# Performance work log

Hardware: AMD Instinct MI355X
Metric: run time of the kernel (lower is better)

## Reference

```python
import jax, jax.numpy as jnp
import numpy as np

B, S, D, H, DI, L = 16, 80, 512, 64, 2048, 6  # batch, seq, d_model, d_lstm(=d_v), d_inner, n_layers
EPS = 1e-6


def _layer_norm(x, g, b):
    m = jnp.mean(x, axis=-1, keepdims=True)
    v = jnp.mean((x - m) ** 2, axis=-1, keepdims=True)
    return (x - m) * jax.lax.rsqrt(v + EPS) * g + b


def _lstm_last(gx, whh):
    # gx: [T, N, 4H] precomputed input-to-gate projections (bias=False LSTM)
    N = gx.shape[1]
    Hh = whh.shape[1]
    init = (jnp.zeros((N, Hh), gx.dtype), jnp.zeros((N, Hh), gx.dtype))

    def step(carry, g_in):
        h, c = carry
        gates = g_in + h @ whh.T  # [N, 4H], torch gate order i,f,g,o
        i, f, g, o = jnp.split(gates, 4, axis=-1)
        c = jax.nn.sigmoid(f) * c + jax.nn.sigmoid(i) * jnp.tanh(g)
        h = jax.nn.sigmoid(o) * jnp.tanh(c)
        return (h, c), None

    (h, _), _ = jax.lax.scan(step, init, gx)
    return h  # [N, H]


def _perm_indices():
    # deterministic janossy permutation: identity with position i swapped to last
    idx = np.arange(S)
    P = np.tile(idx, (S, 1))
    P[idx, idx] = S - 1
    P[idx, S - 1] = idx
    return jnp.asarray(P)  # [S, S]


def _janossy_layer(q, g, b, wih, whh, wfc, P):
    # q: [B, S, D]
    x = _layer_norm(q, g, b)
    # project inputs to gates once, then gather permutations of the projection
    xg = jnp.einsum('bsd,gd->sbg', x, wih)  # [S, B, 4H]
    pg = xg[P]  # [S_i, S_t, B, 4H]: for each output position i, the permuted sequence
    pg = pg.transpose(1, 0, 2, 3).reshape(S, S * B, 4 * H)  # time-major, fold i into batch
    h = _lstm_last(pg, whh)  # [S*B, H]
    h = h.reshape(S, B, H).transpose(1, 0, 2)  # [B, S, H]
    return h @ wfc.T + q  # fc (dropout=identity in eval) + residual


def _ffn(q, g, b, w1, b1, w2, b2):
    x = _layer_norm(q, g, b)
    return jax.nn.relu(x @ w1.T + b1) @ w2.T + b2 + q


def setup_inputs() -> dict:
    key = jax.random.key(0)
    ks = jax.random.split(key, 10)
    n = lambda k, s, sc: jax.random.normal(k, s, jnp.float32) * sc
    return {
        'src_seq': jax.random.normal(ks[0], (B, S, D), jnp.float32),
        'trg_seq': jax.random.normal(ks[1], (B, S, D), jnp.float32),
        'ln1_g': jnp.ones((L, D), jnp.float32),
        'ln1_b': jnp.zeros((L, D), jnp.float32),
        'wih': n(ks[2], (L, 4 * H, D), 0.04),
        'whh': n(ks[3], (L, 4 * H, H), 0.1),
        'wfc': n(ks[4], (L, D, H), 0.05),
        'ln2_g': jnp.ones((L, D), jnp.float32),
        'ln2_b': jnp.zeros((L, D), jnp.float32),
        'w1': n(ks[5], (L, DI, D), 0.03),
        'b1': jnp.zeros((L, DI), jnp.float32),
        'w2': n(ks[6], (L, D, DI), 0.02),
        'b2': jnp.zeros((L, D), jnp.float32),
        'lnf_g': jnp.ones((D,), jnp.float32),
        'lnf_b': jnp.zeros((D,), jnp.float32),
        'wprj': n(ks[7], (1, D), 0.05),
    }


def reference(src_seq, trg_seq, ln1_g, ln1_b, wih, whh, wfc, ln2_g, ln2_b,
              w1, b1, w2, b2, lnf_g, lnf_b, wprj):
    P = _perm_indices()
    x = src_seq
    for l in range(L):  # small fixed layer count
        x = _janossy_layer(x, ln1_g[l], ln1_b[l], wih[l], whh[l], wfc[l], P)
        x = _ffn(x, ln2_g[l], ln2_b[l], w1[l], b1[l], w2[l], b2[l])
    x = _layer_norm(x, lnf_g, lnf_b)
    seq_logit = x @ wprj.T  # [B, S, 1]
    return seq_logit
```

## Files before the change

kernel.cpp:

```cpp
#include <hip/hip_runtime.h>
#include <hip/hip_bf16.h>

#define B_ 16
#define S_ 80
#define D_ 512
#define H_ 64
#define DI_ 2048
#define L_ 6
#define G4H 256
#define NROW (B_ * S_)
#define EPS_ 1e-6f

typedef __attribute__((ext_vector_type(8))) short short8;
typedef __attribute__((ext_vector_type(4))) float f32x4;

__device__ __forceinline__ float sigmoidf_(float x) {
    return __fdividef(1.0f, 1.0f + __expf(-x));
}
__device__ __forceinline__ float tanh_(float x) {
    return __fdividef(2.0f, 1.0f + __expf(-2.0f * x)) - 1.0f;
}
__device__ __forceinline__ short f2bf(float f) {
    __hip_bfloat16 h = __float2bfloat16(f);
    return *reinterpret_cast<short*>(&h);
}

__device__ __forceinline__ void lds_barrier() {
    __asm__ volatile("s_waitcnt lgkmcnt(0)\n\ts_barrier" ::: "memory");
}

__global__ __launch_bounds__(256)
void w2bf_kernel(const float* __restrict__ s, __hip_bfloat16* __restrict__ d, int n4) {
    int i = blockIdx.x * 256 + threadIdx.x;
    if (i < n4) {
        float4 v = reinterpret_cast<const float4*>(s)[i];
        short4 o;
        o.x = f2bf(v.x); o.y = f2bf(v.y); o.z = f2bf(v.z); o.w = f2bf(v.w);
        reinterpret_cast<short4*>(d)[i] = o;
    }
}

__global__ __launch_bounds__(256)
void ln_kernel(const float* __restrict__ x, const float* __restrict__ g,
               const float* __restrict__ b, __hip_bfloat16* __restrict__ out) {
    int row = blockIdx.x;
    int t = threadIdx.x;
    const float* xr = x + (size_t)row * D_;
    float v0 = xr[t], v1 = xr[t + 256];
    __shared__ float ws4[4], qs4[4];
    float s = v0 + v1;
    #pragma unroll
    for (int o = 32; o > 0; o >>= 1) s += __shfl_down(s, o);
    if ((t & 63) == 0) ws4[t >> 6] = s;
    __syncthreads();
    float m = (ws4[0] + ws4[1] + ws4[2] + ws4[3]) * (1.0f / (float)D_);
    float d0 = v0 - m, d1 = v1 - m;
    float q = d0 * d0 + d1 * d1;
    #pragma unroll
    for (int o = 32; o > 0; o >>= 1) q += __shfl_down(q, o);
    if ((t & 63) == 0) qs4[t >> 6] = q;
    __syncthreads();
    float rs = rsqrtf((qs4[0] + qs4[1] + qs4[2] + qs4[3]) * (1.0f / (float)D_) + EPS_);
    __hip_bfloat16* orow = out + (size_t)row * D_;
    orow[t]       = __float2bfloat16(d0 * rs * g[t]       + b[t]);
    orow[t + 256] = __float2bfloat16(d1 * rs * g[t + 256] + b[t + 256]);
}

template<int WITH_BIAS, int WITH_RELU, int WITH_RES, int OUT_MODE>
__global__ __launch_bounds__(256)
void mfma_gemm(const __hip_bfloat16* __restrict__ A, const __hip_bfloat16* __restrict__ W,
               const float* __restrict__ bias, const float* __restrict__ res,
               void* __restrict__ C, int M, int N, int K) {
    const int LDT = 72;
    __shared__ short As[64 * LDT];
    __shared__ short Ws[64 * LDT];

    int tid  = threadIdx.x;
    int wave = tid >> 6, lane = tid & 63;
    int quad = lane >> 4, l16 = lane & 15;
    int m_off = (wave >> 1) * 32, n_off = (wave & 1) * 32;
    int m0 = blockIdx.y * 64, n0 = blockIdx.x * 64;

    int r = tid >> 2, c = tid & 3;
    const short* Ag = reinterpret_cast<const short*>(A);
    const short* Wg = reinterpret_cast<const short*>(W);

    f32x4 acc00 = {0.f,0.f,0.f,0.f}, acc01 = acc00, acc10 = acc00, acc11 = acc00;

    short8 avA[2], avW[2];
    auto load_tile = [&](int k0) {
        const short* arow = &Ag[(size_t)(m0 + r) * K + k0 + c * 16];
        avA[0] = *reinterpret_cast<const short8*>(arow);
        avA[1] = *reinterpret_cast<const short8*>(arow + 8);
        const short* wrow = &Wg[(size_t)(n0 + r) * K + k0 + c * 16];
        avW[0] = *reinterpret_cast<const short8*>(wrow);
        avW[1] = *reinterpret_cast<const short8*>(wrow + 8);
    };

    load_tile(0);
    for (int k0 = 0; k0 < K; k0 += 64) {
        lds_barrier();
        *reinterpret_cast<short8*>(&As[r * LDT + c * 16])     = avA[0];
        *reinterpret_cast<short8*>(&As[r * LDT + c * 16 + 8]) = avA[1];
        *reinterpret_cast<short8*>(&Ws[r * LDT + c * 16])     = avW[0];
        *reinterpret_cast<short8*>(&Ws[r * LDT + c * 16 + 8]) = avW[1];
        lds_barrier();
        if (k0 + 64 < K) load_tile(k0 + 64);

        #pragma unroll
        for (int kc = 0; kc < 2; kc++) {
            short8 a0 = *reinterpret_cast<const short8*>(&As[(m_off + l16) * LDT + kc * 32 + quad * 8]);
            short8 a1 = *reinterpret_cast<const short8*>(&As[(m_off + 16 + l16) * LDT + kc * 32 + quad * 8]);
            short8 b0 = *reinterpret_cast<const short8*>(&Ws[(n_off + l16) * LDT + kc * 32 + quad * 8]);
            short8 b1 = *reinterpret_cast<const short8*>(&Ws[(n_off + 16 + l16) * LDT + kc * 32 + quad * 8]);
            acc00 = __builtin_amdgcn_mfma_f32_16x16x32_bf16(a0, b0, acc00, 0, 0, 0);
            acc01 = __builtin_amdgcn_mfma_f32_16x16x32_bf16(a0, b1, acc01, 0, 0, 0);
            acc10 = __builtin_amdgcn_mfma_f32_16x16x32_bf16(a1, b0, acc10, 0, 0, 0);
            acc11 = __builtin_amdgcn_mfma_f32_16x16x32_bf16(a1, b1, acc11, 0, 0, 0);
        }
    }

    f32x4 accs[2][2] = {{acc00, acc01}, {acc10, acc11}};
    #pragma unroll
    for (int fi = 0; fi < 2; fi++) {
        #pragma unroll
        for (int fj = 0; fj < 2; fj++) {
            int coln = n0 + n_off + fj * 16 + l16;
            float bv = WITH_BIAS ? bias[coln] : 0.0f;
            #pragma unroll
            for (int rr = 0; rr < 4; rr++) {
                int rowm = m0 + m_off + fi * 16 + quad * 4 + rr;
                float v = accs[fi][fj][rr];
                if (WITH_BIAS) v += bv;
                if (WITH_RELU) v = fmaxf(v, 0.0f);
                if (WITH_RES)  v += res[(size_t)rowm * N + coln];
                if (OUT_MODE == 0) {
                    reinterpret_cast<float*>(C)[(size_t)rowm * N + coln] = v;
                } else if (OUT_MODE == 1) {
                    reinterpret_cast<__hip_bfloat16*>(C)[(size_t)rowm * N + coln] = __float2bfloat16(v);
                } else {
                    int b_ = rowm / S_;
                    int s_ = rowm - b_ * S_;
                    int gate = coln >> 6, u = coln & 63;
                    int half = b_ >> 3, slot = b_ & 7;
                    reinterpret_cast<float*>(C)[
                        ((((size_t)(s_ * 2 + half) * 4 + gate) * 64 + u) << 3) + slot] = v;
                }
            }
        }
    }
}

__global__ __launch_bounds__(256)
void lstm_v10_kernel(const float* __restrict__ xg5,
                     const float* __restrict__ whh,
                     __hip_bfloat16* __restrict__ hlast) {
    const int i    = blockIdx.x;
    const int bh   = blockIdx.y;
    const int tid  = threadIdx.x;
    const int wave = tid >> 6, lane = tid & 63;
    const int quad = lane >> 4, l16 = lane & 15;
    const int unit = wave * 16 + l16;

    short8 bfrag[4][2];
    #pragma unroll
    for (int g = 0; g < 4; g++) {
        const float* wr = &whh[(size_t)(g * 64 + unit) * H_];
        #pragma unroll
        for (int kc = 0; kc < 2; kc++) {
            float4 x0 = *(const float4*)(wr + kc * 32 + quad * 8);
            float4 x1 = *(const float4*)(wr + kc * 32 + quad * 8 + 4);
            short8 v;
            v[0] = f2bf(x0.x); v[1] = f2bf(x0.y); v[2] = f2bf(x0.z); v[3] = f2bf(x0.w);
            v[4] = f2bf(x1.x); v[5] = f2bf(x1.y); v[6] = f2bf(x1.z); v[7] = f2bf(x1.w);
            bfrag[g][kc] = v;
        }
    }

    __shared__ __attribute__((aligned(16))) short hsh[2][16][72];
    for (int idx = tid; idx < 2 * 16 * 72; idx += 256)
        reinterpret_cast<short*>(hsh)[idx] = 0;

    float cst[2] = {0.f, 0.f};
    float hvv[2] = {0.f, 0.f};

    size_t xoff[4];
    #pragma unroll
    for (int g = 0; g < 4; g++)
        xoff[g] = ((((size_t)bh * 4 + g) * 64 + unit) << 3) + quad * 2;

    auto xload = [&](float2 (&xv)[4], int t) {
        int s = (t == i) ? (S_ - 1) : ((t == S_ - 1) ? i : t);
        const float* base = xg5 + (size_t)s * 4096;
        #pragma unroll
        for (int g = 0; g < 4; g++)
            xv[g] = *reinterpret_cast<const float2*>(base + xoff[g]);
    };

    float2 xvA[4], xvB[4];
    xload(xvA, 0);
    xload(xvB, 1);

    lds_barrier();

    const f32x4 zacc = {0.f, 0.f, 0.f, 0.f};

    auto stepv = [&](int t, float2 (&xc)[4]) {
        const int pb = t & 1;
        short8 af0 = *reinterpret_cast<const short8*>(&hsh[pb][l16][quad * 8]);
        short8 af1 = *reinterpret_cast<const short8*>(&hsh[pb][l16][32 + quad * 8]);

        f32x4 p0 = __builtin_amdgcn_mfma_f32_16x16x32_bf16(af0, bfrag[0][0], zacc, 0, 0, 0);
        f32x4 q0 = __builtin_amdgcn_mfma_f32_16x16x32_bf16(af1, bfrag[0][1], zacc, 0, 0, 0);
        f32x4 p1 = __builtin_amdgcn_mfma_f32_16x16x32_bf16(af0, bfrag[1][0], zacc, 0, 0, 0);
        f32x4 q1 = __builtin_amdgcn_mfma_f32_16x16x32_bf16(af1, bfrag[1][1], zacc, 0, 0, 0);
        f32x4 p2 = __builtin_amdgcn_mfma_f32_16x16x32_bf16(af0, bfrag[2][0], zacc, 0, 0, 0);
        f32x4 q2 = __builtin_amdgcn_mfma_f32_16x16x32_bf16(af1, bfrag[2][1], zacc, 0, 0, 0);
        f32x4 p3 = __builtin_amdgcn_mfma_f32_16x16x32_bf16(af0, bfrag[3][0], zacc, 0, 0, 0);
        f32x4 q3 = __builtin_amdgcn_mfma_f32_16x16x32_bf16(af1, bfrag[3][1], zacc, 0, 0, 0);

        float gi0 = p0[0] + q0[0] + xc[0].x, gi1 = p0[1] + q0[1] + xc[0].y;
        float gf0 = p1[0] + q1[0] + xc[1].x, gf1 = p1[1] + q1[1] + xc[1].y;
        float gg0 = p2[0] + q2[0] + xc[2].x, gg1 = p2[1] + q2[1] + xc[2].y;
        float go0 = p3[0] + q3[0] + xc[3].x, go1 = p3[1] + q3[1] + xc[3].y;

        if (t + 2 < S_) xload(xc, t + 2);

        {
            float ig = sigmoidf_(gi0);
            float fg = sigmoidf_(gf0);
            float gv = tanh_(gg0);
            float og = sigmoidf_(go0);
            float cc = fg * cst[0] + ig * gv;
            cst[0] = cc;
            float h = og * tanh_(cc);
            hvv[0] = h;
            hsh[pb ^ 1][quad * 4 + 0][unit] = f2bf(h);
        }
        {
            float ig = sigmoidf_(gi1);
            float fg = sigmoidf_(gf1);
            float gv = tanh_(gg1);
            float og = sigmoidf_(go1);
            float cc = fg * cst[1] + ig * gv;
            cst[1] = cc;
            float h = og * tanh_(cc);
            hvv[1] = h;
            hsh[pb ^ 1][quad * 4 + 1][unit] = f2bf(h);
        }
        lds_barrier();
    };

    for (int t = 0; t < S_; t += 2) { stepv(t, xvA); stepv(t + 1, xvB); }

    #pragma unroll
    for (int r = 0; r < 2; r++) {
        int b = bh * 8 + quad * 2 + r;
        hlast[((size_t)b * S_ + i) * H_ + unit] = __float2bfloat16(hvv[r]);
    }
}

__global__ __launch_bounds__(256)
void final_kernel(const float* __restrict__ x, const float* __restrict__ g,
                  const float* __restrict__ b, const float* __restrict__ wprj,
                  float* __restrict__ out) {
    int row = blockIdx.x;
    int t = threadIdx.x;
    const float* xr = x + (size_t)row * D_;
    float v0 = xr[t], v1 = xr[t + 256];
    __shared__ float red[256];
    red[t] = v0 + v1;
    __syncthreads();
    for (int o = 128; o > 0; o >>= 1) { if (t < o) red[t] += red[t + o]; __syncthreads(); }
    float m = red[0] * (1.0f / (float)D_);
    __syncthreads();
    float d0 = v0 - m, d1 = v1 - m;
    red[t] = d0 * d0 + d1 * d1;
    __syncthreads();
    for (int o = 128; o > 0; o >>= 1) { if (t < o) red[t] += red[t + o]; __syncthreads(); }
    float rs = rsqrtf(red[0] * (1.0f / (float)D_) + EPS_);
    __syncthreads();
    float y0 = (d0 * rs * g[t] + b[t]) * wprj[t];
    float y1 = (d1 * rs * g[t + 256] + b[t + 256]) * wprj[t + 256];
    red[t] = y0 + y1;
    __syncthreads();
    for (int o = 128; o > 0; o >>= 1) { if (t < o) red[t] += red[t + o]; __syncthreads(); }
    if (t == 0) out[row] = red[0];
}

extern "C" void kernel_launch(void* const* d_in, const int* in_sizes, int n_in,
                              void* d_out, int out_size, void* d_ws, size_t ws_size,
                              hipStream_t stream) {
    const float* src   = (const float*)d_in[0];
    const float* ln1_g = (const float*)d_in[2];
    const float* ln1_b = (const float*)d_in[3];
    const float* wih   = (const float*)d_in[4];
    const float* whh   = (const float*)d_in[5];
    const float* wfc   = (const float*)d_in[6];
    const float* ln2_g = (const float*)d_in[7];
    const float* ln2_b = (const float*)d_in[8];
    const float* w1    = (const float*)d_in[9];
    const float* b1    = (const float*)d_in[10];
    const float* w2    = (const float*)d_in[11];
    const float* b2    = (const float*)d_in[12];
    const float* lnf_g = (const float*)d_in[13];
    const float* lnf_b = (const float*)d_in[14];
    const float* wprj  = (const float*)d_in[15];
    float* out = (float*)d_out;

    char* ws = (char*)d_ws;
    float* xcur = (float*)ws;                       ws += (size_t)NROW * D_  * 4;
    __hip_bfloat16* lnb = (__hip_bfloat16*)ws;      ws += (size_t)NROW * D_  * 2;
    float* xg5  = (float*)ws;                       ws += (size_t)S_ * 4096  * 4;
    __hip_bfloat16* hb  = (__hip_bfloat16*)ws;      ws += (size_t)NROW * H_  * 2;
    __hip_bfloat16* f1  = (__hip_bfloat16*)ws;      ws += (size_t)NROW * DI_ * 2;
    __hip_bfloat16* wihb = (__hip_bfloat16*)ws;     ws += (size_t)L_ * G4H * D_ * 2;
    __hip_bfloat16* wfcb = (__hip_bfloat16*)ws;     ws += (size_t)L_ * D_ * H_ * 2;
    __hip_bfloat16* w1b  = (__hip_bfloat16*)ws;     ws += (size_t)L_ * DI_ * D_ * 2;
    __hip_bfloat16* w2b  = (__hip_bfloat16*)ws;     ws += (size_t)L_ * D_ * DI_ * 2;

    {
        int n4;
        n4 = L_ * G4H * D_ / 4;
        w2bf_kernel<<<(n4 + 255) / 256, 256, 0, stream>>>(wih, wihb, n4);
        n4 = L_ * D_ * H_ / 4;
        w2bf_kernel<<<(n4 + 255) / 256, 256, 0, stream>>>(wfc, wfcb, n4);
        n4 = L_ * DI_ * D_ / 4;
        w2bf_kernel<<<(n4 + 255) / 256, 256, 0, stream>>>(w1, w1b, n4);
        n4 = L_ * D_ * DI_ / 4;
        w2bf_kernel<<<(n4 + 255) / 256, 256, 0, stream>>>(w2, w2b, n4);
    }

    hipMemcpyAsync(xcur, src, (size_t)NROW * D_ * sizeof(float),
                   hipMemcpyDeviceToDevice, stream);

    for (int l = 0; l < L_; l++) {
        ln_kernel<<<NROW, 256, 0, stream>>>(xcur, ln1_g + (size_t)l * D_,
                                            ln1_b + (size_t)l * D_, lnb);
        mfma_gemm<0, 0, 0, 2><<<dim3(G4H / 64, NROW / 64), 256, 0, stream>>>(
            lnb, wihb + (size_t)l * G4H * D_, nullptr, nullptr, xg5, NROW, G4H, D_);
        lstm_v10_kernel<<<dim3(S_, 2), 256, 0, stream>>>(
            xg5, whh + (size_t)l * G4H * H_, hb);
        mfma_gemm<0, 0, 1, 0><<<dim3(D_ / 64, NROW / 64), 256, 0, stream>>>(
            hb, wfcb + (size_t)l * D_ * H_, nullptr, xcur, xcur, NROW, D_, H_);
        ln_kernel<<<NROW, 256, 0, stream>>>(xcur, ln2_g + (size_t)l * D_,
                                            ln2_b + (size_t)l * D_, lnb);
        mfma_gemm<1, 1, 0, 1><<<dim3(DI_ / 64, NROW / 64), 256, 0, stream>>>(
            lnb, w1b + (size_t)l * DI_ * D_, b1 + (size_t)l * DI_, nullptr, f1, NROW, DI_, D_);
        mfma_gemm<1, 0, 1, 0><<<dim3(D_ / 64, NROW / 64), 256, 0, stream>>>(
            f1, w2b + (size_t)l * D_ * DI_, b2 + (size_t)l * D_, xcur, xcur, NROW, D_, DI_);
    }
    final_kernel<<<NROW, 256, 0, stream>>>(xcur, lnf_g, lnf_b, wprj, out);
}
```

Measured before the change: 710.7 us.

## Fuse LayerNorm into GEMM prologue and use 128-row tiles for FFN1

Removes the standalone LayerNorm kernels. Each GEMM block now computes row mean and variance from fp32 input and normalizes while staging A tiles to LDS. This drops the bf16 LN intermediate buffer and two launches per layer. The FFN1 GEMM also moves to 128-row tiles with 512 threads, so the W tile is shared across more rows. In exchange, every N-block recomputes the row statistics and A is read as fp32, doubling A traffic, and variance now uses the E[x^2]-m^2 form.

```diff
diff --git a/kernel.cpp b/kernel.cpp
--- a/kernel.cpp
+++ b/kernel.cpp
@@ -40,70 +40,106 @@
     }
 }
 
-__global__ __launch_bounds__(256)
-void ln_kernel(const float* __restrict__ x, const float* __restrict__ g,
-               const float* __restrict__ b, __hip_bfloat16* __restrict__ out) {
-    int row = blockIdx.x;
-    int t = threadIdx.x;
-    const float* xr = x + (size_t)row * D_;
-    float v0 = xr[t], v1 = xr[t + 256];
-    __shared__ float ws4[4], qs4[4];
-    float s = v0 + v1;
-    #pragma unroll
-    for (int o = 32; o > 0; o >>= 1) s += __shfl_down(s, o);
-    if ((t & 63) == 0) ws4[t >> 6] = s;
-    __syncthreads();
-    float m = (ws4[0] + ws4[1] + ws4[2] + ws4[3]) * (1.0f / (float)D_);
-    float d0 = v0 - m, d1 = v1 - m;
-    float q = d0 * d0 + d1 * d1;
-    #pragma unroll
-    for (int o = 32; o > 0; o >>= 1) q += __shfl_down(q, o);
-    if ((t & 63) == 0) qs4[t >> 6] = q;
-    __syncthreads();
-    float rs = rsqrtf((qs4[0] + qs4[1] + qs4[2] + qs4[3]) * (1.0f / (float)D_) + EPS_);
-    __hip_bfloat16* orow = out + (size_t)row * D_;
-    orow[t]       = __float2bfloat16(d0 * rs * g[t]       + b[t]);
-    orow[t + 256] = __float2bfloat16(d1 * rs * g[t + 256] + b[t + 256]);
-}
-
-template<int WITH_BIAS, int WITH_RELU, int WITH_RES, int OUT_MODE>
-__global__ __launch_bounds__(256)
-void mfma_gemm(const __hip_bfloat16* __restrict__ A, const __hip_bfloat16* __restrict__ W,
+template<int BM, int WITH_LN, int WITH_BIAS, int WITH_RELU, int WITH_RES, int OUT_MODE>
+__global__ __launch_bounds__(BM * 4)
+void mfma_gemm(const void* __restrict__ Ain, const __hip_bfloat16* __restrict__ W,
+               const float* __restrict__ gamma, const float* __restrict__ beta,
                const float* __restrict__ bias, const float* __restrict__ res,
                void* __restrict__ C, int M, int N, int K) {
     const int LDT = 72;
-    __shared__ short As[64 * LDT];
+    __shared__ short As[BM * LDT];
     __shared__ short Ws[64 * LDT];
 
     int tid  = threadIdx.x;
     int wave = tid >> 6, lane = tid & 63;
     int quad = lane >> 4, l16 = lane & 15;
     int m_off = (wave >> 1) * 32, n_off = (wave & 1) * 32;
-    int m0 = blockIdx.y * 64, n0 = blockIdx.x * 64;
+    int m0 = blockIdx.y * BM, n0 = blockIdx.x * 64;
 
     int r = tid >> 2, c = tid & 3;
-    const short* Ag = reinterpret_cast<const short*>(A);
     const short* Wg = reinterpret_cast<const short*>(W);
+    const short* Ag = reinterpret_cast<const short*>(Ain);
+    const float* Af = reinterpret_cast<const float*>(Ain);
+
+    float mr = 0.f, rsr = 0.f;
+    if constexpr (WITH_LN) {
+        const float* xr = Af + (size_t)(m0 + r) * K + c * 128;
+        float sum = 0.f, sq = 0.f;
+        #pragma unroll 8
+        for (int j = 0; j < 32; j++) {
+            float4 v = *reinterpret_cast<const float4*>(xr + j * 4);
+            sum += v.x + v.y + v.z + v.w;
+            sq  += v.x * v.x + v.y * v.y + v.z * v.z + v.w * v.w;
+        }
+        sum += __shfl_xor(sum, 1); sum += __shfl_xor(sum, 2);
+        sq  += __shfl_xor(sq, 1);  sq  += __shfl_xor(sq, 2);
+        mr  = sum * (1.0f / 512.0f);
+        rsr = rsqrtf(sq * (1.0f / 512.0f) - mr * mr + EPS_);
+    }
 
     f32x4 acc00 = {0.f,0.f,0.f,0.f}, acc01 = acc00, acc10 = acc00, acc11 = acc00;
 
-    short8 avA[2], avW[2];
+    short8 avA[2];
+    float4 avAf[4];
+    short8 avW[2];
+
     auto load_tile = [&](int k0) {
-        const short* arow = &Ag[(size_t)(m0 + r) * K + k0 + c * 16];
-        avA[0] = *reinterpret_cast<const short8*>(arow);
-        avA[1] = *reinterpret_cast<const short8*>(arow + 8);
-        const short* wrow = &Wg[(size_t)(n0 + r) * K + k0 + c * 16];
-        avW[0] = *reinterpret_cast<const short8*>(wrow);
-        avW[1] = *reinterpret_cast<const short8*>(wrow + 8);
+        if constexpr (WITH_LN) {
+            const float* arow = Af + (size_t)(m0 + r) * K + k0 + c * 16;
+            avAf[0] = *reinterpret_cast<const float4*>(arow);
+            avAf[1] = *reinterpret_cast<const float4*>(arow + 4);
+            avAf[2] = *reinterpret_cast<const float4*>(arow + 8);
+            avAf[3] = *reinterpret_cast<const float4*>(arow + 12);
+        } else {
+            const short* arow = &Ag[(size_t)(m0 + r) * K + k0 + c * 16];
+            avA[0] = *reinterpret_cast<const short8*>(arow);
+            avA[1] = *reinterpret_cast<const short8*>(arow + 8);
+        }
+        if constexpr (BM == 64) {
+            const short* wrow = &Wg[(size_t)(n0 + r) * K + k0 + c * 16];
+            avW[0] = *reinterpret_cast<const short8*>(wrow);
+            avW[1] = *reinterpret_cast<const short8*>(wrow + 8);
+        } else {
+            int rw = tid >> 3, cw = tid & 7;
+            const short* wrow = &Wg[(size_t)(n0 + rw) * K + k0 + cw * 8];
+            avW[0] = *reinterpret_cast<const short8*>(wrow);
+        }
+    };
+
+    auto store_tile = [&](int k0) {
+        if constexpr (WITH_LN) {
+            const float* gp = gamma + k0 + c * 16;
+            const float* bp = beta  + k0 + c * 16;
+            short tmp[16];
+            #pragma unroll
+            for (int j = 0; j < 4; j++) {
+                float4 g4 = *reinterpret_cast<const float4*>(gp + j * 4);
+                float4 b4 = *reinterpret_cast<const float4*>(bp + j * 4);
+                float4 a4 = avAf[j];
+                tmp[j * 4 + 0] = f2bf((a4.x - mr) * rsr * g4.x + b4.x);
+                tmp[j * 4 + 1] = f2bf((a4.y - mr) * rsr * g4.y + b4.y);
+                tmp[j * 4 + 2] = f2bf((a4.z - mr) * rsr * g4.z + b4.z);
+                tmp[j * 4 + 3] = f2bf((a4.w - mr) * rsr * g4.w + b4.w);
+            }
+            *reinterpret_cast<short8*>(&As[r * LDT + c * 16])     = *reinterpret_cast<short8*>(&tmp[0]);
+            *reinterpret_cast<short8*>(&As[r * LDT + c * 16 + 8]) = *reinterpret_cast<short8*>(&tmp[8]);
+        } else {
+            *reinterpret_cast<short8*>(&As[r * LDT + c * 16])     = avA[0];
+            *reinterpret_cast<short8*>(&As[r * LDT + c * 16 + 8]) = avA[1];
+        }
+        if constexpr (BM == 64) {
+            *reinterpret_cast<short8*>(&Ws[r * LDT + c * 16])     = avW[0];
+            *reinterpret_cast<short8*>(&Ws[r * LDT + c * 16 + 8]) = avW[1];
+        } else {
+            int rw = tid >> 3, cw = tid & 7;
+            *reinterpret_cast<short8*>(&Ws[rw * LDT + cw * 8]) = avW[0];
+        }
     };
 
     load_tile(0);
     for (int k0 = 0; k0 < K; k0 += 64) {
         lds_barrier();
-        *reinterpret_cast<short8*>(&As[r * LDT + c * 16])     = avA[0];
-        *reinterpret_cast<short8*>(&As[r * LDT + c * 16 + 8]) = avA[1];
-        *reinterpret_cast<short8*>(&Ws[r * LDT + c * 16])     = avW[0];
-        *reinterpret_cast<short8*>(&Ws[r * LDT + c * 16 + 8]) = avW[1];
+        store_tile(k0);
         lds_barrier();
         if (k0 + 64 < K) load_tile(k0 + 64);
 
@@ -310,7 +346,6 @@
 
     char* ws = (char*)d_ws;
     float* xcur = (float*)ws;                       ws += (size_t)NROW * D_  * 4;
-    __hip_bfloat16* lnb = (__hip_bfloat16*)ws;      ws += (size_t)NROW * D_  * 2;
     float* xg5  = (float*)ws;                       ws += (size_t)S_ * 4096  * 4;
     __hip_bfloat16* hb  = (__hip_bfloat16*)ws;      ws += (size_t)NROW * H_  * 2;
     __hip_bfloat16* f1  = (__hip_bfloat16*)ws;      ws += (size_t)NROW * DI_ * 2;
@@ -335,20 +370,22 @@
                    hipMemcpyDeviceToDevice, stream);
 
     for (int l = 0; l < L_; l++) {
-        ln_kernel<<<NROW, 256, 0, stream>>>(xcur, ln1_g + (size_t)l * D_,
-                                            ln1_b + (size_t)l * D_, lnb);
-        mfma_gemm<0, 0, 0, 2><<<dim3(G4H / 64, NROW / 64), 256, 0, stream>>>(
-            lnb, wihb + (size_t)l * G4H * D_, nullptr, nullptr, xg5, NROW, G4H, D_);
+        mfma_gemm<64, 1, 0, 0, 0, 2><<<dim3(G4H / 64, NROW / 64), 256, 0, stream>>>(
+            xcur, wihb + (size_t)l * G4H * D_,
+            ln1_g + (size_t)l * D_, ln1_b + (size_t)l * D_,
+            nullptr, nullptr, xg5, NROW, G4H, D_);
         lstm_v10_kernel<<<dim3(S_, 2), 256, 0, stream>>>(
             xg5, whh + (size_t)l * G4H * H_, hb);
-        mfma_gemm<0, 0, 1, 0><<<dim3(D_ / 64, NROW / 64), 256, 0, stream>>>(
-            hb, wfcb + (size_t)l * D_ * H_, nullptr, xcur, xcur, NROW, D_, H_);
-        ln_kernel<<<NROW, 256, 0, stream>>>(xcur, ln2_g + (size_t)l * D_,
-                                            ln2_b + (size_t)l * D_, lnb);
-        mfma_gemm<1, 1, 0, 1><<<dim3(DI_ / 64, NROW / 64), 256, 0, stream>>>(
-            lnb, w1b + (size_t)l * DI_ * D_, b1 + (size_t)l * DI_, nullptr, f1, NROW, DI_, D_);
-        mfma_gemm<1, 0, 1, 0><<<dim3(D_ / 64, NROW / 64), 256, 0, stream>>>(
-            f1, w2b + (size_t)l * D_ * DI_, b2 + (size_t)l * D_, xcur, xcur, NROW, D_, DI_);
+        mfma_gemm<64, 0, 0, 0, 1, 0><<<dim3(D_ / 64, NROW / 64), 256, 0, stream>>>(
+            hb, wfcb + (size_t)l * D_ * H_, nullptr, nullptr,
+            nullptr, xcur, xcur, NROW, D_, H_);
+        mfma_gemm<128, 1, 1, 1, 0, 1><<<dim3(DI_ / 64, NROW / 128), 512, 0, stream>>>(
+            xcur, w1b + (size_t)l * DI_ * D_,
+            ln2_g + (size_t)l * D_, ln2_b + (size_t)l * D_,
+            b1 + (size_t)l * DI_, nullptr, f1, NROW, DI_, D_);
+        mfma_gemm<64, 0, 1, 0, 1, 0><<<dim3(D_ / 64, NROW / 64), 256, 0, stream>>>(
+            f1, w2b + (size_t)l * D_ * DI_, nullptr, nullptr,
+            b2 + (size_t)l * D_, xcur, xcur, NROW, D_, DI_);
     }
     final_kernel<<<NROW, 256, 0, stream>>>(xcur, lnf_g, lnf_b, wprj, out);
 }
```

Measured after the change: 915.6 us. +28.8%, slower.

## Fuse LSTM output projection, residual and second LayerNorm into LSTM kernel

Applied to the files above, without the earlier changes.

The LSTM kernel now applies the fc projection with MFMA straight from the final hidden state held in shared memory. It then adds the residual into xcur, computes the LayerNorm statistics with a cross-wave reduction, and writes the bf16 normalized rows for the FFN. This removes two kernel launches per layer and the round trip of the hidden-state buffer through global memory. The four weight-conversion launches are also merged into one. The trade-off is extra serial work at the tail of the 160-block LSTM kernel, variance computed as E[x²]-m², and fc weights read uncached by every block.

```diff
diff --git a/kernel.cpp b/kernel.cpp
--- a/kernel.cpp
+++ b/kernel.cpp
@@ -30,14 +30,21 @@
 }
 
 __global__ __launch_bounds__(256)
-void w2bf_kernel(const float* __restrict__ s, __hip_bfloat16* __restrict__ d, int n4) {
+void w2bf_all_kernel(const float* __restrict__ s0, int n0, __hip_bfloat16* __restrict__ d0,
+                     const float* __restrict__ s1, int n1, __hip_bfloat16* __restrict__ d1,
+                     const float* __restrict__ s2, int n2, __hip_bfloat16* __restrict__ d2,
+                     const float* __restrict__ s3, int n3, __hip_bfloat16* __restrict__ d3) {
     int i = blockIdx.x * 256 + threadIdx.x;
-    if (i < n4) {
-        float4 v = reinterpret_cast<const float4*>(s)[i];
-        short4 o;
-        o.x = f2bf(v.x); o.y = f2bf(v.y); o.z = f2bf(v.z); o.w = f2bf(v.w);
-        reinterpret_cast<short4*>(d)[i] = o;
-    }
+    const float* s; __hip_bfloat16* d;
+    if (i < n0)      { s = s0; d = d0; }
+    else if ((i -= n0) < n1) { s = s1; d = d1; }
+    else if ((i -= n1) < n2) { s = s2; d = d2; }
+    else if ((i -= n2) < n3) { s = s3; d = d3; }
+    else return;
+    float4 v = reinterpret_cast<const float4*>(s)[i];
+    short4 o;
+    o.x = f2bf(v.x); o.y = f2bf(v.y); o.z = f2bf(v.z); o.w = f2bf(v.w);
+    reinterpret_cast<short4*>(d)[i] = o;
 }
 
 __global__ __launch_bounds__(256)
@@ -152,9 +159,13 @@
 }
 
 __global__ __launch_bounds__(256)
-void lstm_v10_kernel(const float* __restrict__ xg5,
-                     const float* __restrict__ whh,
-                     __hip_bfloat16* __restrict__ hlast) {
+void lstm_fc_kernel(const float* __restrict__ xg5,
+                    const float* __restrict__ whh,
+                    const __hip_bfloat16* __restrict__ wfcb,
+                    const float* __restrict__ g2,
+                    const float* __restrict__ b2v,
+                    float* __restrict__ xcur,
+                    __hip_bfloat16* __restrict__ lnb) {
     const int i    = blockIdx.x;
     const int bh   = blockIdx.y;
     const int tid  = threadIdx.x;
@@ -178,11 +189,11 @@
     }
 
     __shared__ __attribute__((aligned(16))) short hsh[2][16][72];
+    __shared__ float sred[4][4][2][2];
     for (int idx = tid; idx < 2 * 16 * 72; idx += 256)
         reinterpret_cast<short*>(hsh)[idx] = 0;
 
     float cst[2] = {0.f, 0.f};
-    float hvv[2] = {0.f, 0.f};
 
     size_t xoff[4];
     #pragma unroll
@@ -233,9 +244,7 @@
             float og = sigmoidf_(go0);
             float cc = fg * cst[0] + ig * gv;
             cst[0] = cc;
-            float h = og * tanh_(cc);
-            hvv[0] = h;
-            hsh[pb ^ 1][quad * 4 + 0][unit] = f2bf(h);
+            hsh[pb ^ 1][quad * 4 + 0][unit] = f2bf(og * tanh_(cc));
         }
         {
             float ig = sigmoidf_(gi1);
@@ -244,19 +253,79 @@
             float og = sigmoidf_(go1);
             float cc = fg * cst[1] + ig * gv;
             cst[1] = cc;
-            float h = og * tanh_(cc);
-            hvv[1] = h;
-            hsh[pb ^ 1][quad * 4 + 1][unit] = f2bf(h);
+            hsh[pb ^ 1][quad * 4 + 1][unit] = f2bf(og * tanh_(cc));
         }
         lds_barrier();
     };
 
     for (int t = 0; t < S_; t += 2) { stepv(t, xvA); stepv(t + 1, xvB); }
 
-    #pragma unroll
-    for (int r = 0; r < 2; r++) {
-        int b = bh * 8 + quad * 2 + r;
-        hlast[((size_t)b * S_ + i) * H_ + unit] = __float2bfloat16(hvv[r]);
+    {
+        const short* wf = reinterpret_cast<const short*>(wfcb);
+        short8 af0 = *reinterpret_cast<const short8*>(&hsh[0][l16][quad * 8]);
+        short8 af1 = *reinterpret_cast<const short8*>(&hsh[0][l16][32 + quad * 8]);
+
+        f32x4 facc[8];
+        #pragma unroll
+        for (int nn = 0; nn < 8; nn++) {
+            int col16 = (wave * 8 + nn) * 16 + l16;
+            short8 w0 = *reinterpret_cast<const short8*>(&wf[(size_t)col16 * H_ + quad * 8]);
+            short8 w1 = *reinterpret_cast<const short8*>(&wf[(size_t)col16 * H_ + 32 + quad * 8]);
+            f32x4 a = __builtin_amdgcn_mfma_f32_16x16x32_bf16(af0, w0, zacc, 0, 0, 0);
+            facc[nn] = __builtin_amdgcn_mfma_f32_16x16x32_bf16(af1, w1, a, 0, 0, 0);
+        }
+
+        float xn[8][2];
+        float ssum[2] = {0.f, 0.f}, sq[2] = {0.f, 0.f};
+        #pragma unroll
+        for (int nn = 0; nn < 8; nn++) {
+            int col = (wave * 8 + nn) * 16 + l16;
+            #pragma unroll
+            for (int rr = 0; rr < 2; rr++) {
+                int b = bh * 8 + quad * 2 + rr;
+                size_t adr = ((size_t)b * S_ + i) * D_ + col;
+                float v = facc[nn][rr] + xcur[adr];
+                xn[nn][rr] = v;
+                xcur[adr] = v;
+                ssum[rr] += v;
+                sq[rr]   += v * v;
+            }
+        }
+        #pragma unroll
+        for (int m = 1; m < 16; m <<= 1) {
+            ssum[0] += __shfl_xor(ssum[0], m); ssum[1] += __shfl_xor(ssum[1], m);
+            sq[0]   += __shfl_xor(sq[0], m);   sq[1]   += __shfl_xor(sq[1], m);
+        }
+        if (l16 == 0) {
+            #pragma unroll
+            for (int rr = 0; rr < 2; rr++) {
+                sred[wave][quad][rr][0] = ssum[rr];
+                sred[wave][quad][rr][1] = sq[rr];
+            }
+        }
+        lds_barrier();
+        float mmean[2], rstd[2];
+        #pragma unroll
+        for (int rr = 0; rr < 2; rr++) {
+            float s = sred[0][quad][rr][0] + sred[1][quad][rr][0]
+                    + sred[2][quad][rr][0] + sred[3][quad][rr][0];
+            float q = sred[0][quad][rr][1] + sred[1][quad][rr][1]
+                    + sred[2][quad][rr][1] + sred[3][quad][rr][1];
+            float m = s * (1.0f / (float)D_);
+            mmean[rr] = m;
+            rstd[rr]  = rsqrtf(q * (1.0f / (float)D_) - m * m + EPS_);
+        }
+        #pragma unroll
+        for (int nn = 0; nn < 8; nn++) {
+            int col = (wave * 8 + nn) * 16 + l16;
+            float gv = g2[col], bv = b2v[col];
+            #pragma unroll
+            for (int rr = 0; rr < 2; rr++) {
+                int b = bh * 8 + quad * 2 + rr;
+                lnb[((size_t)b * S_ + i) * D_ + col] =
+                    __float2bfloat16((xn[nn][rr] - mmean[rr]) * rstd[rr] * gv + bv);
+            }
+        }
     }
 }
 
@@ -312,7 +381,6 @@
     float* xcur = (float*)ws;                       ws += (size_t)NROW * D_  * 4;
     __hip_bfloat16* lnb = (__hip_bfloat16*)ws;      ws += (size_t)NROW * D_  * 2;
     float* xg5  = (float*)ws;                       ws += (size_t)S_ * 4096  * 4;
-    __hip_bfloat16* hb  = (__hip_bfloat16*)ws;      ws += (size_t)NROW * H_  * 2;
     __hip_bfloat16* f1  = (__hip_bfloat16*)ws;      ws += (size_t)NROW * DI_ * 2;
     __hip_bfloat16* wihb = (__hip_bfloat16*)ws;     ws += (size_t)L_ * G4H * D_ * 2;
     __hip_bfloat16* wfcb = (__hip_bfloat16*)ws;     ws += (size_t)L_ * D_ * H_ * 2;
@@ -320,15 +388,13 @@
     __hip_bfloat16* w2b  = (__hip_bfloat16*)ws;     ws += (size_t)L_ * D_ * DI_ * 2;
 
     {
-        int n4;
-        n4 = L_ * G4H * D_ / 4;
-        w2bf_kernel<<<(n4 + 255) / 256, 256, 0, stream>>>(wih, wihb, n4);
-        n4 = L_ * D_ * H_ / 4;
-        w2bf_kernel<<<(n4 + 255) / 256, 256, 0, stream>>>(wfc, wfcb, n4);
-        n4 = L_ * DI_ * D_ / 4;
-        w2bf_kernel<<<(n4 + 255) / 256, 256, 0, stream>>>(w1, w1b, n4);
-        n4 = L_ * D_ * DI_ / 4;
-        w2bf_kernel<<<(n4 + 255) / 256, 256, 0, stream>>>(w2, w2b, n4);
+        int n0 = L_ * G4H * D_ / 4;
+        int n1 = L_ * D_ * H_ / 4;
+        int n2 = L_ * DI_ * D_ / 4;
+        int n3 = L_ * D_ * DI_ / 4;
+        int total = n0 + n1 + n2 + n3;
+        w2bf_all_kernel<<<(total + 255) / 256, 256, 0, stream>>>(
+            wih, n0, wihb, wfc, n1, wfcb, w1, n2, w1b, w2, n3, w2b);
     }
 
     hipMemcpyAsync(xcur, src, (size_t)NROW * D_ * sizeof(float),
@@ -339,12 +405,9 @@
                                             ln1_b + (size_t)l * D_, lnb);
         mfma_gemm<0, 0, 0, 2><<<dim3(G4H / 64, NROW / 64), 256, 0, stream>>>(
             lnb, wihb + (size_t)l * G4H * D_, nullptr, nullptr, xg5, NROW, G4H, D_);
-        lstm_v10_kernel<<<dim3(S_, 2), 256, 0, stream>>>(
-            xg5, whh + (size_t)l * G4H * H_, hb);
-        mfma_gemm<0, 0, 1, 0><<<dim3(D_ / 64, NROW / 64), 256, 0, stream>>>(
-            hb, wfcb + (size_t)l * D_ * H_, nullptr, xcur, xcur, NROW, D_, H_);
-        ln_kernel<<<NROW, 256, 0, stream>>>(xcur, ln2_g + (size_t)l * D_,
-                                            ln2_b + (size_t)l * D_, lnb);
+        lstm_fc_kernel<<<dim3(S_, 2), 256, 0, stream>>>(
+            xg5, whh + (size_t)l * G4H * H_, wfcb + (size_t)l * D_ * H_,
+            ln2_g + (size_t)l * D_, ln2_b + (size_t)l * D_, xcur, lnb);
         mfma_gemm<1, 1, 0, 1><<<dim3(DI_ / 64, NROW / 64), 256, 0, stream>>>(
             lnb, w1b + (size_t)l * DI_ * D_, b1 + (size_t)l * DI_, nullptr, f1, NROW, DI_, D_);
         mfma_gemm<1, 0, 1, 0><<<dim3(D_ / 64, NROW / 64), 256, 0, stream>>>(
```

Result: faster. 692.9 us, median of 2 (-2.5%).
